# Optimization experiments

Hardware: AMD Instinct MI355X
Metric: run time of the kernel (lower is better)

## Reference

```python
import jax, jax.numpy as jnp
import numpy as np

N = 8192
D = 256
DENSITY = 0.02  # ~164 neighbors per node


def setup_inputs() -> dict:
    key = jax.random.key(0)
    k1, k2, k3, k4 = jax.random.split(key, 4)
    inputs = jax.random.normal(k1, (N, D), dtype=jnp.float32)
    vals = jax.random.uniform(k2, (N, N), dtype=jnp.float32, minval=0.1, maxval=1.0)
    mask = jax.random.uniform(k3, (N, N), dtype=jnp.float32) < DENSITY
    adj = jnp.where(mask, vals, 0.0)
    H_v = 0.1 * jax.random.normal(k4, (D, 1), dtype=jnp.float32)
    return {"inputs": inputs, "adj": adj, "H_v": H_v}


def reference(inputs, adj, H_v):
    # scores[j] = inputs[j] . H_v  -> sparse values v_ij = adj_ij * scores[j]
    scores = jnp.squeeze(inputs @ H_v, -1)            # [N]
    mask = adj != 0.0                                  # nonzero pattern of SparseTensor
    logits = adj * scores[None, :]                     # [N, N]
    neg = jnp.asarray(jnp.finfo(logits.dtype).min, logits.dtype)
    logits = jnp.where(mask, logits, neg)
    # sparse softmax: normalize only over nonzero entries per row
    m = jnp.max(logits, axis=1, keepdims=True)
    e = jnp.where(mask, jnp.exp(logits - m), 0.0)
    s = jnp.sum(e, axis=1, keepdims=True)
    weights = e / jnp.where(s > 0, s, 1.0)             # empty rows -> all-zero weights
    # sparse_tensor_dense_matmul(weights, inputs)
    return weights @ inputs                            # [N, D]
```

## Files before the change

kernel.cpp:

```cpp
#include <hip/hip_runtime.h>

#define NN 8192
#define DD 256
#define RT 32
#define KC 128
#define NCHUNK (NN / KC)

typedef float v4f __attribute__((ext_vector_type(4)));
typedef short short8 __attribute__((ext_vector_type(8)));
typedef float f32x4 __attribute__((ext_vector_type(4)));
typedef unsigned short u16x4 __attribute__((ext_vector_type(4)));
typedef unsigned short u16x8 __attribute__((ext_vector_type(8)));

__device__ __forceinline__ unsigned short f2bf_rne(float x) {
    unsigned u = __float_as_uint(x);
    u += 0x7fffu + ((u >> 16) & 1u);
    return (unsigned short)(u >> 16);
}
__device__ __forceinline__ float bf_to_f(unsigned short b) {
    return __uint_as_float((unsigned)b << 16);
}

__global__ __launch_bounds__(256) void scores_kernel(const float* __restrict__ inputs,
                                                     const float* __restrict__ Hv,
                                                     float* __restrict__ scores) {
    int wave = threadIdx.x >> 6;
    int lane = threadIdx.x & 63;
    int row  = blockIdx.x * 4 + wave;
    if (row >= NN) return;
    float4 v = ((const float4*)(inputs + (size_t)row * DD))[lane];
    float4 h = ((const float4*)Hv)[lane];
    float s = v.x * h.x + v.y * h.y + v.z * h.z + v.w * h.w;
    #pragma unroll
    for (int off = 32; off > 0; off >>= 1) s += __shfl_down(s, off, 64);
    if (lane == 0) scores[row] = s;
}

#define XP 258
__global__ __launch_bounds__(256) void xt_kernel(const float* __restrict__ inputs,
                                                 unsigned short* __restrict__ xt) {
    __shared__ unsigned short sx[64 * XP];
    const int tid = threadIdx.x;
    const int k0  = blockIdx.x * 64;
    #pragma unroll
    for (int r = 0; r < 16; ++r) {
        int row = r * 4 + (tid >> 6);
        int col = (tid & 63) * 4;
        float4 v = *(const float4*)(inputs + (size_t)(k0 + row) * DD + col);
        u16x4 w;
        w[0] = f2bf_rne(v.x); w[1] = f2bf_rne(v.y); w[2] = f2bf_rne(v.z); w[3] = f2bf_rne(v.w);
        *(u16x4*)&sx[row * XP + col] = w;
    }
    __syncthreads();
    #pragma unroll
    for (int rep = 0; rep < 8; ++rep) {
        int n  = rep * 32 + (tid >> 3);
        int kg = (tid & 7) * 8;
        u16x8 w;
        #pragma unroll
        for (int j = 0; j < 8; ++j) w[j] = sx[(kg + j) * XP + n];
        *(u16x8*)(xt + (size_t)n * NN + k0 + kg) = w;
    }
}

__global__ __launch_bounds__(512, 1) void spmm_kernel(const float* __restrict__ adj,
                                                      const unsigned short* __restrict__ xt,
                                                      const float* __restrict__ scores,
                                                      float* __restrict__ out) {
    __shared__ unsigned short sE[2][RT * KC];
    __shared__ float s_den[RT];

    const int tid  = threadIdx.x;
    const int lane = tid & 63;
    const int wave = tid >> 6;
    const int q    = lane >> 4;
    const int m16  = lane & 15;
    const int row0 = blockIdx.x * RT;

    const int lrow = tid >> 4;
    const int kgb  = tid & 15;
    const int kg   = kgb * 8;
    const float* arow = adj + (size_t)(row0 + lrow) * NN;

    f32x4 acc[2][2] = {};
    float den = 0.f;

    v4f a0 = __builtin_nontemporal_load((const v4f*)(arow + kg));
    v4f a1 = __builtin_nontemporal_load((const v4f*)(arow + kg + 4));
    float4 s0 = *(const float4*)(scores + kg);
    float4 s1 = *(const float4*)(scores + kg + 4);

    for (int c = 0; c < NCHUNK; ++c) {
        const int cn = (c + 1 < NCHUNK ? c + 1 : c) * KC;
        v4f na0 = __builtin_nontemporal_load((const v4f*)(arow + cn + kg));
        v4f na1 = __builtin_nontemporal_load((const v4f*)(arow + cn + kg + 4));
        float4 ns0 = *(const float4*)(scores + cn + kg);
        float4 ns1 = *(const float4*)(scores + cn + kg + 4);

        float af[8] = { a0.x, a0.y, a0.z, a0.w, a1.x, a1.y, a1.z, a1.w };
        float sf[8] = { s0.x, s0.y, s0.z, s0.w, s1.x, s1.y, s1.z, s1.w };
        u16x8 ev;
        #pragma unroll
        for (int i = 0; i < 8; ++i) {
            float e = (af[i] != 0.f) ? __expf(af[i] * sf[i]) : 0.f;
            unsigned short b = f2bf_rne(e);
            ev[i] = b;
            den += bf_to_f(b);
        }
        *(u16x8*)&sE[c & 1][lrow * KC + ((kgb ^ (lrow & 15)) * 8)] = ev;
        __syncthreads();

        const unsigned short* Eb = sE[c & 1];
        short8 afr[2][4];
        #pragma unroll
        for (int mt = 0; mt < 2; ++mt)
            #pragma unroll
            for (int kh = 0; kh < 4; ++kh) {
                int m = mt * 16 + m16;
                afr[mt][kh] = *(const short8*)&Eb[m * KC + (((kh * 4 + q) ^ m16) * 8)];
            }
        short8 bfr[2][4];
        #pragma unroll
        for (int nt = 0; nt < 2; ++nt)
            #pragma unroll
            for (int kh = 0; kh < 4; ++kh) {
                int n = wave * 32 + nt * 16 + m16;
                bfr[nt][kh] = *(const short8*)(xt + (size_t)n * NN + c * KC + kh * 32 + q * 8);
            }
        #pragma unroll
        for (int mt = 0; mt < 2; ++mt)
            #pragma unroll
            for (int nt = 0; nt < 2; ++nt)
                #pragma unroll
                for (int kh = 0; kh < 4; ++kh)
                    acc[mt][nt] = __builtin_amdgcn_mfma_f32_16x16x32_bf16(
                        afr[mt][kh], bfr[nt][kh], acc[mt][nt], 0, 0, 0);

        a0 = na0; a1 = na1; s0 = ns0; s1 = ns1;
    }

    #pragma unroll
    for (int d = 1; d < 16; d <<= 1) den += __shfl_xor(den, d, 64);
    if ((tid & 15) == 0) s_den[lrow] = den;
    __syncthreads();

    #pragma unroll
    for (int mt = 0; mt < 2; ++mt)
        #pragma unroll
        for (int nt = 0; nt < 2; ++nt)
            #pragma unroll
            for (int r = 0; r < 4; ++r) {
                int rr = mt * 16 + q * 4 + r;
                float dn = s_den[rr];
                float v = (dn > 0.f) ? acc[mt][nt][r] / dn : 0.f;
                out[(size_t)(row0 + rr) * DD + wave * 32 + nt * 16 + m16] = v;
            }
}

__global__ __launch_bounds__(256) void attn_fallback(const float* __restrict__ adj,
                                                     const float* __restrict__ inputs,
                                                     const float* __restrict__ scores,
                                                     float* __restrict__ out) {
    __shared__ int   s_j[1024];
    __shared__ float s_e[1024];
    __shared__ int   s_cnt;
    const int row = blockIdx.x;
    const int tid = threadIdx.x;
    const float* arow = adj + (size_t)row * NN;
    float acc = 0.f, ssum = 0.f;
    for (int base = 0; base < NN; base += 1024) {
        if (tid == 0) s_cnt = 0;
        __syncthreads();
        float4 a = ((const float4*)(arow + base))[tid];
        int j0 = base + tid * 4;
        if (a.x != 0.f) { int k = atomicAdd(&s_cnt, 1); s_j[k] = j0 + 0; s_e[k] = __expf(a.x * scores[j0 + 0]); }
        if (a.y != 0.f) { int k = atomicAdd(&s_cnt, 1); s_j[k] = j0 + 1; s_e[k] = __expf(a.y * scores[j0 + 1]); }
        if (a.z != 0.f) { int k = atomicAdd(&s_cnt, 1); s_j[k] = j0 + 2; s_e[k] = __expf(a.z * scores[j0 + 2]); }
        if (a.w != 0.f) { int k = atomicAdd(&s_cnt, 1); s_j[k] = j0 + 3; s_e[k] = __expf(a.w * scores[j0 + 3]); }
        __syncthreads();
        int c = s_cnt;
        for (int k = 0; k < c; ++k) {
            float e = s_e[k];
            acc  += e * inputs[(size_t)s_j[k] * DD + tid];
            ssum += e;
        }
        __syncthreads();
    }
    out[(size_t)row * DD + tid] = (ssum > 0.f) ? acc / ssum : 0.f;
}

extern "C" void kernel_launch(void* const* d_in, const int* in_sizes, int n_in,
                              void* d_out, int out_size, void* d_ws, size_t ws_size,
                              hipStream_t stream) {
    const float* inputs = (const float*)d_in[0];
    const float* adj    = (const float*)d_in[1];
    const float* Hv     = (const float*)d_in[2];
    float* out = (float*)d_out;

    char* ws = (char*)d_ws;
    float*          scores = (float*)ws;
    unsigned short* xt     = (unsigned short*)(ws + 32768);

    const size_t need = 32768 + (size_t)DD * NN * sizeof(unsigned short);

    scores_kernel<<<NN / 4, 256, 0, stream>>>(inputs, Hv, scores);
    if (ws_size >= need) {
        xt_kernel<<<NN / 64, 256, 0, stream>>>(inputs, xt);
        spmm_kernel<<<NN / RT, 512, 0, stream>>>(adj, xt, scores, out);
    } else {
        attn_fallback<<<NN, 256, 0, stream>>>(adj, inputs, scores, out);
    }
}
```

Measured before the change: 464.2 us.

## Split K across two blocks and prepack X into MFMA-fragment layout

The dense SpMM now splits the K dimension into two halves, launching twice as many blocks. Each block writes partial numerators and denominators to workspace, and a new reduce kernel combines them and normalises. X^T is also repacked so each wave's B-fragment loads are contiguous 16-byte-per-lane reads instead of strided row accesses. The split raises parallelism over 256 blocks on a 256-CU device, at the cost of an extra kernel and 16 MB of partial-result traffic. The launch-bounds change to 4 blocks per CU may also pressure registers.

Result: faster. 399.5 us (-13.9%).

```diff
diff --git a/kernel.cpp b/kernel.cpp
--- a/kernel.cpp
+++ b/kernel.cpp
@@ -4,7 +4,9 @@
 #define DD 256
 #define RT 32
 #define KC 128
-#define NCHUNK (NN / KC)
+#define KS 2
+#define KRANGE (NN / KS)
+#define NCH (KRANGE / KC)
 
 typedef float v4f __attribute__((ext_vector_type(4)));
 typedef short short8 __attribute__((ext_vector_type(8)));
@@ -37,8 +39,8 @@
 }
 
 #define XP 258
-__global__ __launch_bounds__(256) void xt_kernel(const float* __restrict__ inputs,
-                                                 unsigned short* __restrict__ xt) {
+__global__ __launch_bounds__(256) void xtp_kernel(const float* __restrict__ inputs,
+                                                  unsigned short* __restrict__ xtp) {
     __shared__ unsigned short sx[64 * XP];
     const int tid = threadIdx.x;
     const int k0  = blockIdx.x * 64;
@@ -53,49 +55,57 @@
     }
     __syncthreads();
     #pragma unroll
-    for (int rep = 0; rep < 8; ++rep) {
-        int n  = rep * 32 + (tid >> 3);
-        int kg = (tid & 7) * 8;
+    for (int r = 0; r < 8; ++r) {
+        int rid  = r * 256 + tid;
+        int lane = rid & 63;
+        int t    = (rid >> 6) & 15;
+        int kcl  = rid >> 10;
+        int n    = t * 16 + (lane & 15);
+        int kl   = kcl * 32 + (lane >> 4) * 8;
         u16x8 w;
         #pragma unroll
-        for (int j = 0; j < 8; ++j) w[j] = sx[(kg + j) * XP + n];
-        *(u16x8*)(xt + (size_t)n * NN + k0 + kg) = w;
-    }
-}
-
-__global__ __launch_bounds__(512, 1) void spmm_kernel(const float* __restrict__ adj,
-                                                      const unsigned short* __restrict__ xt,
+        for (int j = 0; j < 8; ++j) w[j] = sx[(kl + j) * XP + n];
+        size_t kcg = (size_t)(k0 >> 5) + kcl;
+        *(u16x8*)(xtp + (((size_t)t * 256 + kcg) * 64 + lane) * 8) = w;
+    }
+}
+
+__global__ __launch_bounds__(512, 4) void spmm_kernel(const float* __restrict__ adj,
+                                                      const unsigned short* __restrict__ xtp,
                                                       const float* __restrict__ scores,
-                                                      float* __restrict__ out) {
+                                                      float* __restrict__ pc,
+                                                      float* __restrict__ pd) {
     __shared__ unsigned short sE[2][RT * KC];
-    __shared__ float s_den[RT];
-
     const int tid  = threadIdx.x;
     const int lane = tid & 63;
     const int wave = tid >> 6;
     const int q    = lane >> 4;
     const int m16  = lane & 15;
-    const int row0 = blockIdx.x * RT;
+
+    const int ks   = blockIdx.x & (KS - 1);
+    const int mb   = blockIdx.x >> 1;
+    const int row0 = mb * RT;
+    const int kbase = ks * KRANGE;
 
     const int lrow = tid >> 4;
     const int kgb  = tid & 15;
     const int kg   = kgb * 8;
-    const float* arow = adj + (size_t)(row0 + lrow) * NN;
+    const float* arow = adj + (size_t)(row0 + lrow) * NN + kbase;
 
     f32x4 acc[2][2] = {};
     float den = 0.f;
 
     v4f a0 = __builtin_nontemporal_load((const v4f*)(arow + kg));
     v4f a1 = __builtin_nontemporal_load((const v4f*)(arow + kg + 4));
-    float4 s0 = *(const float4*)(scores + kg);
-    float4 s1 = *(const float4*)(scores + kg + 4);
-
-    for (int c = 0; c < NCHUNK; ++c) {
-        const int cn = (c + 1 < NCHUNK ? c + 1 : c) * KC;
+    float4 s0 = *(const float4*)(scores + kbase + kg);
+    float4 s1 = *(const float4*)(scores + kbase + kg + 4);
+
+    for (int c = 0; c < NCH; ++c) {
+        const int cn = (c + 1 < NCH ? c + 1 : c) * KC;
         v4f na0 = __builtin_nontemporal_load((const v4f*)(arow + cn + kg));
         v4f na1 = __builtin_nontemporal_load((const v4f*)(arow + cn + kg + 4));
-        float4 ns0 = *(const float4*)(scores + cn + kg);
-        float4 ns1 = *(const float4*)(scores + cn + kg + 4);
+        float4 ns0 = *(const float4*)(scores + kbase + cn + kg);
+        float4 ns1 = *(const float4*)(scores + kbase + cn + kg + 4);
 
         float af[8] = { a0.x, a0.y, a0.z, a0.w, a1.x, a1.y, a1.z, a1.w };
         float sf[8] = { s0.x, s0.y, s0.z, s0.w, s1.x, s1.y, s1.z, s1.w };
@@ -110,23 +120,23 @@
         *(u16x8*)&sE[c & 1][lrow * KC + ((kgb ^ (lrow & 15)) * 8)] = ev;
         __syncthreads();
 
+        const size_t kcg0 = (size_t)((kbase + c * KC) >> 5);
+        short8 bfr[2][4];
+        #pragma unroll
+        for (int nt = 0; nt < 2; ++nt) {
+            const size_t t = (size_t)(wave * 2 + nt);
+            #pragma unroll
+            for (int kh = 0; kh < 4; ++kh)
+                bfr[nt][kh] = *(const short8*)(xtp + ((t * 256 + kcg0 + kh) * 64 + lane) * 8);
+        }
         const unsigned short* Eb = sE[c & 1];
         short8 afr[2][4];
         #pragma unroll
         for (int mt = 0; mt < 2; ++mt)
             #pragma unroll
-            for (int kh = 0; kh < 4; ++kh) {
-                int m = mt * 16 + m16;
-                afr[mt][kh] = *(const short8*)&Eb[m * KC + (((kh * 4 + q) ^ m16) * 8)];
-            }
-        short8 bfr[2][4];
-        #pragma unroll
-        for (int nt = 0; nt < 2; ++nt)
-            #pragma unroll
-            for (int kh = 0; kh < 4; ++kh) {
-                int n = wave * 32 + nt * 16 + m16;
-                bfr[nt][kh] = *(const short8*)(xt + (size_t)n * NN + c * KC + kh * 32 + q * 8);
-            }
+            for (int kh = 0; kh < 4; ++kh)
+                afr[mt][kh] = *(const short8*)&Eb[(mt * 16 + m16) * KC + (((kh * 4 + q) ^ m16) * 8)];
+
         #pragma unroll
         for (int mt = 0; mt < 2; ++mt)
             #pragma unroll
@@ -141,9 +151,9 @@
 
     #pragma unroll
     for (int d = 1; d < 16; d <<= 1) den += __shfl_xor(den, d, 64);
-    if ((tid & 15) == 0) s_den[lrow] = den;
-    __syncthreads();
-
+    if ((tid & 15) == 0) pd[(size_t)ks * NN + row0 + lrow] = den;
+
+    float* pcb = pc + ((size_t)ks * NN + row0) * DD;
     #pragma unroll
     for (int mt = 0; mt < 2; ++mt)
         #pragma unroll
@@ -151,10 +161,18 @@
             #pragma unroll
             for (int r = 0; r < 4; ++r) {
                 int rr = mt * 16 + q * 4 + r;
-                float dn = s_den[rr];
-                float v = (dn > 0.f) ? acc[mt][nt][r] / dn : 0.f;
-                out[(size_t)(row0 + rr) * DD + wave * 32 + nt * 16 + m16] = v;
+                pcb[(size_t)rr * DD + wave * 32 + nt * 16 + m16] = acc[mt][nt][r];
             }
+}
+
+__global__ __launch_bounds__(256) void reduce_kernel(const float* __restrict__ pc,
+                                                     const float* __restrict__ pd,
+                                                     float* __restrict__ out) {
+    const int row = blockIdx.x;
+    const int tid = threadIdx.x;
+    float d = pd[row] + pd[NN + row];
+    float v = pc[(size_t)row * DD + tid] + pc[((size_t)NN + row) * DD + tid];
+    out[(size_t)row * DD + tid] = (d > 0.f) ? v / d : 0.f;
 }
 
 __global__ __launch_bounds__(256) void attn_fallback(const float* __restrict__ adj,
@@ -199,14 +217,18 @@
 
     char* ws = (char*)d_ws;
     float*          scores = (float*)ws;
-    unsigned short* xt     = (unsigned short*)(ws + 32768);
-
-    const size_t need = 32768 + (size_t)DD * NN * sizeof(unsigned short);
+    unsigned short* xtp    = (unsigned short*)(ws + 32768);
+    float*          pd     = (float*)(ws + 32768 + (size_t)NN * DD * 2);
+    float*          pc     = (float*)(ws + 32768 + (size_t)NN * DD * 2 + KS * NN * 4);
+
+    const size_t need = 32768 + (size_t)NN * DD * 2 + (size_t)KS * NN * 4
+                      + (size_t)KS * NN * DD * 4;
 
     scores_kernel<<<NN / 4, 256, 0, stream>>>(inputs, Hv, scores);
     if (ws_size >= need) {
-        xt_kernel<<<NN / 64, 256, 0, stream>>>(inputs, xt);
-        spmm_kernel<<<NN / RT, 512, 0, stream>>>(adj, xt, scores, out);
+        xtp_kernel<<<NN / 64, 256, 0, stream>>>(inputs, xtp);
+        spmm_kernel<<<(NN / RT) * KS, 512, 0, stream>>>(adj, xtp, scores, pc, pd);
+        reduce_kernel<<<NN, 256, 0, stream>>>(pc, pd, out);
     } else {
         attn_fallback<<<NN, 256, 0, stream>>>(adj, inputs, scores, out);
     }
```
